# Optimization experiments

Hardware: AMD Instinct MI355X
Metric: run time of the kernel (lower is better)

## Reference

```python
import jax, jax.numpy as jnp
import numpy as np

# Config matching init_kwargs: kernel_size=1, patch_size=21, stride=1,
# padding=0, dilation=1, dilation_patch=2  -> patch-based branch.
PATCH = 21
DIL_P = 2
STRIDE = 1
HALF = PATCH // 2          # 10
PAD = HALF * DIL_P         # 20


def setup_inputs() -> dict:
    key = jax.random.key(0)
    k1, k2 = jax.random.split(key)
    B, C, H, W = 8, 256, 96, 96
    input1 = jax.random.normal(k1, (B, C, H, W), dtype=jnp.float32)
    input2 = jax.random.normal(k2, (B, C, H, W), dtype=jnp.float32)
    return {"input1": input1, "input2": input2}


def reference(input1, input2):
    # Faithful to the torch module's _correlation_patch_based: both inputs are
    # sampled at the SAME shifted location, so
    #   out[b, ph, pw, y, x] = sum_c in1[b,c,y',x'] * in2[b,c,y',x']
    # with y' = y*stride + (ph-HALF)*DIL_P (zero if out of bounds).
    B, C, H, W = input1.shape
    out_h = (H - 1) // STRIDE + 1
    out_w = (W - 1) // STRIDE + 1

    # Per-pixel dot product over channels: [B, H, W]
    D = jnp.sum(input1 * input2, axis=1)
    # Zero-pad so out-of-bounds shifts read zeros
    Dp = jnp.pad(D, ((0, 0), (PAD, PAD), (PAD, PAD)))

    shifts = (jnp.arange(PATCH) - HALF) * DIL_P            # [P]
    ys = jnp.arange(out_h) * STRIDE                        # [oh]
    xs = jnp.arange(out_w) * STRIDE                        # [ow]
    yi = shifts[:, None] + ys[None, :] + PAD               # [P, oh]
    xi = shifts[:, None] + xs[None, :] + PAD               # [P, ow]

    # Gather: [B, P, P, oh, ow]
    out = Dp[:, yi[:, None, :, None], xi[None, :, None, :]]
    return out.reshape(B, PATCH * PATCH, out_h, out_w)
```

## Files before the change

kernel.cpp:

```cpp
#include <hip/hip_runtime.h>

constexpr int B = 8, C = 256, H = 96, W = 96;
constexpr int HW = H * W;
constexpr int NPIX = B * HW;
constexpr int PATCH = 21;
constexpr int HALF = PATCH / 2;
constexpr int DIL = 2;
constexpr int P2 = PATCH * PATCH;

__global__ __launch_bounds__(256) void dot_kernel(const float* __restrict__ a,
                                                  const float* __restrict__ b,
                                                  float* __restrict__ D) {
    int pix = blockIdx.x * blockDim.x + threadIdx.x;
    if (pix >= NPIX) return;
    int bb = pix / HW;
    int hw = pix - bb * HW;
    const float* pa = a + (size_t)bb * C * HW + hw;
    const float* pb = b + (size_t)bb * C * HW + hw;
    float acc0 = 0.f, acc1 = 0.f, acc2 = 0.f, acc3 = 0.f;
    #pragma unroll 4
    for (int c = 0; c < C; c += 4) {
        float a0 = pa[(size_t)(c + 0) * HW];
        float a1 = pa[(size_t)(c + 1) * HW];
        float a2 = pa[(size_t)(c + 2) * HW];
        float a3 = pa[(size_t)(c + 3) * HW];
        float b0 = pb[(size_t)(c + 0) * HW];
        float b1 = pb[(size_t)(c + 1) * HW];
        float b2 = pb[(size_t)(c + 2) * HW];
        float b3 = pb[(size_t)(c + 3) * HW];
        acc0 = fmaf(a0, b0, acc0);
        acc1 = fmaf(a1, b1, acc1);
        acc2 = fmaf(a2, b2, acc2);
        acc3 = fmaf(a3, b3, acc3);
    }
    D[pix] = (acc0 + acc1) + (acc2 + acc3);
}

__global__ __launch_bounds__(256) void scatter_kernel(const float* __restrict__ D,
                                                      float* __restrict__ out) {
    constexpr int W4 = W / 4;
    constexpr int TOTAL = B * P2 * H * W4;
    int tid = blockIdx.x * blockDim.x + threadIdx.x;
    if (tid >= TOTAL) return;

    int x4 = tid % W4;
    int t  = tid / W4;
    int y  = t % H;  t /= H;
    int p  = t % P2; t /= P2;
    int bb = t;

    int py = p / PATCH;
    int px = p - py * PATCH;
    int sy = y + (py - HALF) * DIL;
    int x0 = x4 * 4;
    int sx0 = x0 + (px - HALF) * DIL;

    float4 v = make_float4(0.f, 0.f, 0.f, 0.f);
    if (sy >= 0 && sy < H) {
        const float* row = D + (size_t)(bb * H + sy) * W;
        if (sx0 >= 0 && sx0 + 3 < W) {
            float2 lo = *(const float2*)(row + sx0);
            float2 hi = *(const float2*)(row + sx0 + 2);
            v = make_float4(lo.x, lo.y, hi.x, hi.y);
        } else {
            float* pv = &v.x;
            #pragma unroll
            for (int i = 0; i < 4; ++i) {
                int sx = sx0 + i;
                if (sx >= 0 && sx < W) pv[i] = row[sx];
            }
        }
    }
    reinterpret_cast<float4*>(out)[tid] = v;
}

extern "C" void kernel_launch(void* const* d_in, const int* in_sizes, int n_in,
                              void* d_out, int out_size, void* d_ws, size_t ws_size,
                              hipStream_t stream) {
    const float* in1 = (const float*)d_in[0];
    const float* in2 = (const float*)d_in[1];
    float* out = (float*)d_out;
    float* D = (float*)d_ws;

    {
        int threads = 256;
        int blocks = (NPIX + threads - 1) / threads;
        dot_kernel<<<blocks, threads, 0, stream>>>(in1, in2, D);
    }
    {
        constexpr int TOTAL = B * P2 * H * (W / 4);
        int threads = 256;
        int blocks = (TOTAL + threads - 1) / threads;
        scatter_kernel<<<blocks, threads, 0, stream>>>(D, out);
    }
}
```

Before: 243.6 us.

## Split channel reduction across threads with float4 loads and widen scatter to 8 outputs

The dot kernel now gives each block 64 pixels and splits the 256 channels across 16 thread rows. Each thread reads float4 vectors over 16 channels, and the partial sums are combined with a shared-memory tree reduction. This is meant to give more parallelism and wider loads than one thread per pixel looping over all channels, at the cost of barriers and shared memory. The scatter kernel now writes 8 outputs per thread with two float4 stores instead of 4, which cuts index arithmetic and the thread count but halves the number of threads.

Measured after the change: 247.5 us. About the same (+1.6%).

```diff
diff --git a/kernel.cpp b/kernel.cpp
--- a/kernel.cpp
+++ b/kernel.cpp
@@ -11,40 +11,55 @@
 __global__ __launch_bounds__(256) void dot_kernel(const float* __restrict__ a,
                                                   const float* __restrict__ b,
                                                   float* __restrict__ D) {
-    int pix = blockIdx.x * blockDim.x + threadIdx.x;
-    if (pix >= NPIX) return;
-    int bb = pix / HW;
-    int hw = pix - bb * HW;
-    const float* pa = a + (size_t)bb * C * HW + hw;
-    const float* pb = b + (size_t)bb * C * HW + hw;
-    float acc0 = 0.f, acc1 = 0.f, acc2 = 0.f, acc3 = 0.f;
-    #pragma unroll 4
-    for (int c = 0; c < C; c += 4) {
-        float a0 = pa[(size_t)(c + 0) * HW];
-        float a1 = pa[(size_t)(c + 1) * HW];
-        float a2 = pa[(size_t)(c + 2) * HW];
-        float a3 = pa[(size_t)(c + 3) * HW];
-        float b0 = pb[(size_t)(c + 0) * HW];
-        float b1 = pb[(size_t)(c + 1) * HW];
-        float b2 = pb[(size_t)(c + 2) * HW];
-        float b3 = pb[(size_t)(c + 3) * HW];
-        acc0 = fmaf(a0, b0, acc0);
-        acc1 = fmaf(a1, b1, acc1);
-        acc2 = fmaf(a2, b2, acc2);
-        acc3 = fmaf(a3, b3, acc3);
+    __shared__ float4 red[16][16];
+    const int tx = threadIdx.x;
+    const int ty = threadIdx.y;
+    const int blk = blockIdx.x;
+    const int pix0 = blk * 64;
+    const int bb = pix0 / HW;
+    const int hw0 = pix0 - bb * HW;
+
+    const int c0 = ty * 16;
+    const float4* pa = (const float4*)(a + ((size_t)bb * C + c0) * HW + hw0) + tx;
+    const float4* pb = (const float4*)(b + ((size_t)bb * C + c0) * HW + hw0) + tx;
+    constexpr size_t CH_STRIDE = HW / 4;
+
+    float4 acc = make_float4(0.f, 0.f, 0.f, 0.f);
+    #pragma unroll 8
+    for (int k = 0; k < 16; ++k) {
+        float4 av = pa[k * CH_STRIDE];
+        float4 bv = pb[k * CH_STRIDE];
+        acc.x = fmaf(av.x, bv.x, acc.x);
+        acc.y = fmaf(av.y, bv.y, acc.y);
+        acc.z = fmaf(av.z, bv.z, acc.z);
+        acc.w = fmaf(av.w, bv.w, acc.w);
     }
-    D[pix] = (acc0 + acc1) + (acc2 + acc3);
+    red[ty][tx] = acc;
+    __syncthreads();
+    #pragma unroll
+    for (int s = 8; s > 0; s >>= 1) {
+        if (ty < s) {
+            float4 o = red[ty + s][tx];
+            float4 m = red[ty][tx];
+            m.x += o.x; m.y += o.y; m.z += o.z; m.w += o.w;
+            red[ty][tx] = m;
+        }
+        __syncthreads();
+    }
+    if (ty == 0) {
+        ((float4*)(D + (size_t)bb * HW + hw0))[tx] = red[0][tx];
+    }
 }
 
 __global__ __launch_bounds__(256) void scatter_kernel(const float* __restrict__ D,
                                                       float* __restrict__ out) {
-    constexpr int W4 = W / 4;
-    constexpr int TOTAL = B * P2 * H * W4;
+    constexpr int W8 = W / 8;
+    constexpr int TOTAL = B * P2 * H * W8;
     int tid = blockIdx.x * blockDim.x + threadIdx.x;
     if (tid >= TOTAL) return;
 
-    int x4 = tid % W4;
-    int t  = tid / W4;
+    int x8 = tid % W8;
+    int t  = tid / W8;
     int y  = t % H;  t /= H;
     int p  = t % P2; t /= P2;
     int bb = t;
@@ -52,26 +67,38 @@
     int py = p / PATCH;
     int px = p - py * PATCH;
     int sy = y + (py - HALF) * DIL;
-    int x0 = x4 * 4;
+    int x0 = x8 * 8;
     int sx0 = x0 + (px - HALF) * DIL;
 
-    float4 v = make_float4(0.f, 0.f, 0.f, 0.f);
+    float4 v0 = make_float4(0.f, 0.f, 0.f, 0.f);
+    float4 v1 = make_float4(0.f, 0.f, 0.f, 0.f);
     if (sy >= 0 && sy < H) {
         const float* row = D + (size_t)(bb * H + sy) * W;
-        if (sx0 >= 0 && sx0 + 3 < W) {
-            float2 lo = *(const float2*)(row + sx0);
-            float2 hi = *(const float2*)(row + sx0 + 2);
-            v = make_float4(lo.x, lo.y, hi.x, hi.y);
+        if (sx0 >= 0 && sx0 + 7 < W) {
+            float2 a0 = *(const float2*)(row + sx0);
+            float2 a1 = *(const float2*)(row + sx0 + 2);
+            float2 a2 = *(const float2*)(row + sx0 + 4);
+            float2 a3 = *(const float2*)(row + sx0 + 6);
+            v0 = make_float4(a0.x, a0.y, a1.x, a1.y);
+            v1 = make_float4(a2.x, a2.y, a3.x, a3.y);
         } else {
-            float* pv = &v.x;
+            float* pv0 = &v0.x;
+            float* pv1 = &v1.x;
             #pragma unroll
             for (int i = 0; i < 4; ++i) {
                 int sx = sx0 + i;
-                if (sx >= 0 && sx < W) pv[i] = row[sx];
+                if (sx >= 0 && sx < W) pv0[i] = row[sx];
+            }
+            #pragma unroll
+            for (int i = 0; i < 4; ++i) {
+                int sx = sx0 + 4 + i;
+                if (sx >= 0 && sx < W) pv1[i] = row[sx];
             }
         }
     }
-    reinterpret_cast<float4*>(out)[tid] = v;
+    float4* o = reinterpret_cast<float4*>(out) + (size_t)tid * 2;
+    o[0] = v0;
+    o[1] = v1;
 }
 
 extern "C" void kernel_launch(void* const* d_in, const int* in_sizes, int n_in,
@@ -83,12 +110,12 @@
     float* D = (float*)d_ws;
 
     {
-        int threads = 256;
-        int blocks = (NPIX + threads - 1) / threads;
+        dim3 threads(16, 16);
+        int blocks = NPIX / 64;
         dot_kernel<<<blocks, threads, 0, stream>>>(in1, in2, D);
     }
     {
-        constexpr int TOTAL = B * P2 * H * (W / 4);
+        constexpr int TOTAL = B * P2 * H * (W / 8);
         int threads = 256;
         int blocks = (TOTAL + threads - 1) / threads;
         scatter_kernel<<<blocks, threads, 0, stream>>>(D, out);
```
